# Kernel tuning notes

Measured on AMD Instinct MI355X. Metric: run time of the kernel, lower is better.

## Reference

```python
import jax, jax.numpy as jnp
import numpy as np

B = 128
N = 65536          # total nodes across batched subgraphs
E = 1048576        # total edges
CLIP_DIM = 768
PD = 512           # projection_dim


def setup_inputs() -> dict:
    key = jax.random.key(0)
    ks = jax.random.split(key, 20)
    s = 0.02
    return {
        # CLIP-encoded features (clip encoders treated as upstream feature extractors)
        "image_features": jax.random.normal(ks[0], (B, CLIP_DIM), jnp.float32),
        "text_features": jax.random.normal(ks[1], (B, CLIP_DIM), jnp.float32),
        "answer": jax.random.uniform(ks[2], (B,), jnp.float32),
        # batched subgraph (X_fixed rows already gathered, as in extract_subgraph_batch)
        "x_nodes": jax.random.normal(ks[3], (N, PD), jnp.float32),
        "edge_index": jax.random.randint(ks[4], (2, E), 0, N, jnp.int32),
        "batch_vec": jnp.sort(jax.random.randint(ks[5], (N,), 0, B, jnp.int32)),
        # image/text projections (clip_dim != projection_dim -> Linear)
        "W_img": jax.random.normal(ks[6], (CLIP_DIM, PD), jnp.float32) * s,
        "b_img": jnp.zeros((PD,), jnp.float32),
        "W_txt": jax.random.normal(ks[7], (CLIP_DIM, PD), jnp.float32) * s,
        "b_txt": jnp.zeros((PD,), jnp.float32),
        # implicit classifier: Linear(2*PD, PD) -> ReLU -> Linear(PD, 1)
        "W1": jax.random.normal(ks[8], (2 * PD, PD), jnp.float32) * s,
        "b1": jnp.zeros((PD,), jnp.float32),
        "W2": jax.random.normal(ks[9], (PD, 1), jnp.float32) * s,
        "b2": jnp.zeros((1,), jnp.float32),
        # GCNConv(PD, PD)
        "Wg": jax.random.normal(ks[10], (PD, PD), jnp.float32) * s,
        "bg": jnp.zeros((PD,), jnp.float32),
        # symbolic classifier: Linear(PD, PD) -> ReLU -> Linear(PD, 1)
        "Ws1": jax.random.normal(ks[11], (PD, PD), jnp.float32) * s,
        "bs1": jnp.zeros((PD,), jnp.float32),
        "Ws2": jax.random.normal(ks[12], (PD, 1), jnp.float32) * s,
        "bs2": jnp.zeros((1,), jnp.float32),
    }


def gcn_conv(x, edge_index, W, b):
    """PyG GCNConv: h = W x; add self-loops; sym-normalized sum aggregation."""
    n = x.shape[0]
    h = x @ W                                     # [N, PD] dense GEMM
    loop = jnp.arange(n, dtype=edge_index.dtype)
    src = jnp.concatenate([edge_index[0], loop])  # [E+N]
    dst = jnp.concatenate([edge_index[1], loop])
    deg = jax.ops.segment_sum(jnp.ones_like(dst, dtype=h.dtype), dst, num_segments=n)
    dis = jax.lax.rsqrt(deg)                      # deg >= 1 (self loops)
    norm = dis[src] * dis[dst]                    # [E+N]
    out = jax.ops.segment_sum(h[src] * norm[:, None], dst, num_segments=n)
    return out + b


def reference(image_features, text_features, answer, x_nodes, edge_index, batch_vec,
              W_img, b_img, W_txt, b_txt, W1, b1, W2, b2,
              Wg, bg, Ws1, bs1, Ws2, bs2):
    # ---- implicit branch (MedicalVQAModel.forward) ----
    img = image_features @ W_img + b_img          # [B, PD]
    txt = text_features @ W_txt + b_txt           # [B, PD]
    combined = jnp.concatenate([img, txt], axis=-1)
    h = jax.nn.relu(combined @ W1 + b1)           # dropout p=0.1 inactive (eval)
    y_implicit = (h @ W2 + b2)[:, 0]              # [B]

    # ---- symbolic branch: GCN over batched subgraphs ----
    x = gcn_conv(x_nodes, edge_index, Wg, bg)
    x = jax.nn.relu(x)                            # dropout p=0.8 inactive (eval)
    bv = batch_vec.astype(jnp.int32)
    sums = jax.ops.segment_sum(x, bv, num_segments=B)          # [B, PD]
    cnts = jax.ops.segment_sum(jnp.ones((x.shape[0],), x.dtype), bv, num_segments=B)
    graph_features = sums / jnp.maximum(cnts, 1.0)[:, None]    # global_mean_pool
    hs = jax.nn.relu(graph_features @ Ws1 + bs1)
    y_symbolic = (hs @ Ws2 + bs2)[:, 0]           # [B]

    logits = jnp.maximum(y_implicit, y_symbolic)
    # BCEWithLogits (mean): log(1+e^l) - l*y
    loss = jnp.mean(jnp.logaddexp(0.0, logits) - logits * answer)
    return (logits, loss)
```

## Files before the change

### kernel.cpp

```cpp
#include <hip/hip_runtime.h>
#include <stdint.h>

#define N_NODES 65536
#define N_EDGES 1048576
#define BATCH   128
#define PD      512
#define CLIPD   768

typedef __attribute__((ext_vector_type(4))) float f32x4;
typedef __attribute__((ext_vector_type(2))) float f32x2;
typedef __attribute__((ext_vector_type(4))) int   i32x4;

__device__ __forceinline__ unsigned short f2b(float f) {
    uint32_t u = __float_as_uint(f);
    return (unsigned short)((u + 0x7fffu + ((u >> 16) & 1u)) >> 16);
}

__device__ __forceinline__ uint32_t pk_bf16(float lo, float hi) {
    uint32_t r;
    asm("v_cvt_pk_bf16_f32 %0, %1, %2" : "=v"(r) : "v"(lo), "v"(hi));
    return r;
}

__device__ __forceinline__ uint32_t pk_fp4(float x, float y, float one) {
    uint32_t r = 0;
    asm("v_cvt_scalef32_pk_fp4_f32 %0, %1, %2, %3" : "+v"(r) : "v"(x), "v"(y), "v"(one));
    return r;
}
__device__ __forceinline__ f32x2 upk_fp4(uint32_t b, float one) {
    f32x2 r;
    asm("v_cvt_scalef32_pk_f32_fp4 %0, %1, %2" : "=v"(r) : "v"(b), "v"(one));
    return r;
}

__global__ void k_wgt(const float* __restrict__ Wg, unsigned short* __restrict__ WgT,
                      const int* __restrict__ bv, int* __restrict__ cnts) {
    __shared__ float tile[32][33];
    int kb = blockIdx.x * 32, nb = blockIdx.y * 32;
    int tx = threadIdx.x, ty = threadIdx.y;
    if (kb == 0 && nb == 0) {
        int tid = ty * 32 + tx;
        if (tid < BATCH) {
            int lo = 0, hi = N_NODES;
            while (lo < hi) { int m = (lo + hi) >> 1; if (bv[m] < tid) lo = m + 1; else hi = m; }
            int lo2 = lo, hi2 = N_NODES;
            while (lo2 < hi2) { int m = (lo2 + hi2) >> 1; if (bv[m] < tid + 1) lo2 = m + 1; else hi2 = m; }
            cnts[tid] = lo2 - lo;
        }
    }
    tile[ty][tx] = Wg[(size_t)(kb + ty) * PD + nb + tx];
    __syncthreads();
    WgT[(size_t)(nb + ty) * PD + kb + tx] = f2b(tile[tx][ty]);
}

__global__ void k_deg(const int* __restrict__ ei, int* __restrict__ deg) {
    int e = blockIdx.x * 256 + threadIdx.x;
    atomicAdd(&deg[ei[N_EDGES + e]], 1);
}

__global__ void k_scan(const int* __restrict__ deg, int* __restrict__ row_ptr,
                       float* __restrict__ dis) {
    __shared__ int wsum[16];
    const int t = threadIdx.x;
    const int w = t >> 6, l = t & 63;
    const int base = w * 4096;
    int s = 0;
    for (int i = 0; i < 64; ++i) s += deg[base + i * 64 + l];
#pragma unroll
    for (int off = 1; off < 64; off <<= 1) s += __shfl_xor(s, off);
    if (l == 0) wsum[w] = s;
    __syncthreads();
    int carry = 0;
    for (int i = 0; i < 16; ++i) carry += (i < w) ? wsum[i] : 0;
    int idx = base + l;
    int d = deg[idx];
    for (int i = 0; i < 64; ++i) {
        int dn = 0;
        if (i < 63) dn = deg[idx + 64];
        int v = d;
        int inc = v;
#pragma unroll
        for (int off = 1; off < 64; off <<= 1) {
            int n = __shfl_up(inc, off);
            if (l >= off) inc += n;
        }
        row_ptr[idx] = carry + inc - v;
        dis[idx] = rsqrtf((float)(d + 1));
        carry += __shfl(inc, 63);
        idx += 64;
        d = dn;
    }
    if (t == 1023) row_ptr[N_NODES] = carry;
}

__global__ void k_scatter(const int* __restrict__ ei, const int* __restrict__ row_ptr,
                          int* __restrict__ fill, int* __restrict__ srcs) {
    int e = blockIdx.x * 256 + threadIdx.x;
    int d = ei[N_EDGES + e];
    int pos = row_ptr[d] + atomicAdd(&fill[d], 1);
    srcs[pos] = ei[e];
}

__device__ __forceinline__ void mfma16(f32x4& acc, i32x4 a, i32x4 b) {
    asm("v_mfma_f32_16x16x32_bf16 %0, %1, %2, %0" : "+v"(acc) : "v"(a), "v"(b));
}

__global__ __launch_bounds__(256) void k_gemm(const float* __restrict__ X,
                                              const unsigned short* __restrict__ WgT,
                                              const float* __restrict__ dis,
                                              uint8_t* __restrict__ hn4) {
    __shared__ __align__(16) unsigned short As[128 * 32];
    __shared__ __align__(16) unsigned short Bs[256 * 32];
    const int m0 = blockIdx.x * 128;
    const int n0 = blockIdx.y * 256;
    const int t = threadIdx.x;
    const int lane = t & 63, w = t >> 6;
    const int wr = w >> 1, wc = w & 1;
    const int g = lane >> 4, lr = lane & 15;

    f32x4 acc[4][8] = {};

    for (int k0 = 0; k0 < PD; k0 += 32) {
        __syncthreads();
#pragma unroll
        for (int it = 0; it < 4; ++it) {
            int idx = it * 256 + t;
            int r = idx >> 3, kc = (idx & 7) * 4;
            float4 v = *(const float4*)&X[(size_t)(m0 + r) * PD + k0 + kc];
            uint2 o;
            o.x = pk_bf16(v.x, v.y);
            o.y = pk_bf16(v.z, v.w);
            *(uint2*)&As[r * 32 + kc] = o;
        }
#pragma unroll
        for (int it = 0; it < 4; ++it) {
            int idx = it * 256 + t;
            int r = idx >> 2, kc = (idx & 3) * 8;
            *(uint4*)&Bs[r * 32 + kc] = *(const uint4*)&WgT[(size_t)(n0 + r) * PD + k0 + kc];
        }
        __syncthreads();

        i32x4 a[4], b[8];
#pragma unroll
        for (int i = 0; i < 4; ++i) a[i] = *(const i32x4*)&As[(wr * 64 + i * 16 + lr) * 32 + g * 8];
#pragma unroll
        for (int j = 0; j < 8; ++j) b[j] = *(const i32x4*)&Bs[(wc * 128 + j * 16 + lr) * 32 + g * 8];
#pragma unroll
        for (int i = 0; i < 4; ++i)
#pragma unroll
            for (int j = 0; j < 8; ++j) mfma16(acc[i][j], a[i], b[j]);
    }
    asm volatile("s_nop 7\n s_nop 7\n s_nop 7\n s_nop 7");

    const float one = 1.0f;
#pragma unroll
    for (int i = 0; i < 4; ++i) {
#pragma unroll
        for (int r = 0; r < 4; ++r) {
            int row = m0 + wr * 64 + i * 16 + g * 4 + r;
            float dd = dis[row] * 16.f;
#pragma unroll
            for (int jh = 0; jh < 4; ++jh) {
                float x = acc[i][2 * jh][r] * dd;
                float y = acc[i][2 * jh + 1][r] * dd;
                uint32_t p = pk_fp4(x, y, one);
                hn4[(size_t)row * 256 + (n0 >> 1) + wc * 64 + jh * 16 + lr] = (uint8_t)p;
            }
        }
    }
}

#define NPB 8
__global__ __launch_bounds__(256) void k_agg(const uint8_t* __restrict__ hn4,
                                             const float* __restrict__ dis,
                                             const float* __restrict__ bg,
                                             const int* __restrict__ row_ptr,
                                             const int* __restrict__ srcs,
                                             const int* __restrict__ bv,
                                             float* __restrict__ sums) {
    const int t = threadIdx.x;
    const int c0 = (t >> 4) * 32 + (t & 15);
    const int c1 = c0 + 16;
    const int node0 = blockIdx.x * NPB;
    const float bg0 = bg[c0], bg1 = bg[c1];
    const float one = 1.0f;
    float s0 = 0.f, s1 = 0.f;
    int curb = bv[node0];
    for (int ni = 0; ni < NPB; ++ni) {
        int node = node0 + ni;
        int b = bv[node];
        if (b != curb) {
            atomicAdd(&sums[(size_t)curb * PD + c0], s0);
            atomicAdd(&sums[(size_t)curb * PD + c1], s1);
            s0 = s1 = 0.f;
            curb = b;
        }
        float a0 = 0.f, a1 = 0.f;
        int beg = row_ptr[node], end = row_ptr[node + 1];
        int e = beg;
        for (; e + 16 <= end; e += 16) {
            int sn[16];
#pragma unroll
            for (int q = 0; q < 16; ++q) sn[q] = srcs[e + q];
            uint32_t v[16];
#pragma unroll
            for (int q = 0; q < 16; ++q)
                v[q] = hn4[(size_t)sn[q] * 256 + t];
#pragma unroll
            for (int q = 0; q < 16; ++q) {
                f32x2 f = upk_fp4(v[q], one);
                a0 += f[0];
                a1 += f[1];
            }
        }
        for (; e + 8 <= end; e += 8) {
            int sn[8];
#pragma unroll
            for (int q = 0; q < 8; ++q) sn[q] = srcs[e + q];
            uint32_t v[8];
#pragma unroll
            for (int q = 0; q < 8; ++q)
                v[q] = hn4[(size_t)sn[q] * 256 + t];
#pragma unroll
            for (int q = 0; q < 8; ++q) {
                f32x2 f = upk_fp4(v[q], one);
                a0 += f[0];
                a1 += f[1];
            }
        }
        for (; e < end; ++e) {
            f32x2 f = upk_fp4(hn4[(size_t)srcs[e] * 256 + t], one);
            a0 += f[0];
            a1 += f[1];
        }
        {
            f32x2 f = upk_fp4(hn4[(size_t)node * 256 + t], one);
            a0 += f[0];
            a1 += f[1];
        }
        float dd = dis[node] * 0.0625f;
        a0 = fmaxf(fmaf(a0, dd, bg0), 0.f);
        a1 = fmaxf(fmaf(a1, dd, bg1), 0.f);
        s0 += a0;
        s1 += a1;
    }
    atomicAdd(&sums[(size_t)curb * PD + c0], s0);
    atomicAdd(&sums[(size_t)curb * PD + c1], s1);
}

__device__ __forceinline__ void lin_part_core(const float* __restrict__ a,
                                              const float* __restrict__ wp,
                                              float* __restrict__ P, int slot, int c0) {
    float acc0 = 0.f, acc1 = 0.f, acc2 = 0.f, acc3 = 0.f;
    float acc4 = 0.f, acc5 = 0.f, acc6 = 0.f, acc7 = 0.f;
#pragma unroll 4
    for (int k = 0; k < 256; k += 8) {
        float a0 = a[k + 0], a1 = a[k + 1], a2 = a[k + 2], a3 = a[k + 3];
        float a4 = a[k + 4], a5 = a[k + 5], a6 = a[k + 6], a7 = a[k + 7];
        float2 w0 = *(const float2*)&wp[(size_t)(k + 0) * PD];
        float2 w1 = *(const float2*)&wp[(size_t)(k + 1) * PD];
        float2 w2 = *(const float2*)&wp[(size_t)(k + 2) * PD];
        float2 w3 = *(const float2*)&wp[(size_t)(k + 3) * PD];
        float2 w4 = *(const float2*)&wp[(size_t)(k + 4) * PD];
        float2 w5 = *(const float2*)&wp[(size_t)(k + 5) * PD];
        float2 w6 = *(const float2*)&wp[(size_t)(k + 6) * PD];
        float2 w7 = *(const float2*)&wp[(size_t)(k + 7) * PD];
        acc0 = fmaf(a0, w0.x, acc0); acc1 = fmaf(a0, w0.y, acc1);
        acc2 = fmaf(a1, w1.x, acc2); acc3 = fmaf(a1, w1.y, acc3);
        acc4 = fmaf(a2, w2.x, acc4); acc5 = fmaf(a2, w2.y, acc5);
        acc6 = fmaf(a3, w3.x, acc6); acc7 = fmaf(a3, w3.y, acc7);
        acc0 = fmaf(a4, w4.x, acc0); acc1 = fmaf(a4, w4.y, acc1);
        acc2 = fmaf(a5, w5.x, acc2); acc3 = fmaf(a5, w5.y, acc3);
        acc4 = fmaf(a6, w6.x, acc4); acc5 = fmaf(a6, w6.y, acc5);
        acc6 = fmaf(a7, w7.x, acc6); acc7 = fmaf(a7, w7.y, acc7);
    }
    P[(size_t)slot * PD + c0] = (acc0 + acc2) + (acc4 + acc6);
    P[(size_t)slot * PD + c0 + 1] = (acc1 + acc3) + (acc5 + acc7);
}

__global__ __launch_bounds__(256) void k_lin_part(const float* __restrict__ A,
                                                  const float* __restrict__ W,
                                                  float* __restrict__ P, int K) {
    const int row = blockIdx.x, kc = blockIdx.y, c0 = threadIdx.x * 2;
    lin_part_core(A + (size_t)row * K + kc * 256, W + (size_t)kc * 256 * PD + c0,
                  P, row * 8 + kc, c0);
}

__global__ __launch_bounds__(256) void k_lin_part_it(const float* __restrict__ IMG,
                                                     const float* __restrict__ TXT,
                                                     const float* __restrict__ Wi,
                                                     const float* __restrict__ Wt,
                                                     float* __restrict__ P) {
    const int row = blockIdx.x, kc = blockIdx.y, c0 = threadIdx.x * 2;
    const float* A = (kc < 3) ? IMG : TXT;
    const float* W = (kc < 3) ? Wi : Wt;
    const int sub = (kc < 3) ? kc : kc - 3;
    lin_part_core(A + (size_t)row * CLIPD + sub * 256, W + (size_t)sub * 256 * PD + c0,
                  P, row * 8 + kc, c0);
}

__global__ __launch_bounds__(256) void k_lin_red_it(const float* __restrict__ P,
                                                    const float* __restrict__ bi,
                                                    const float* __restrict__ bt,
                                                    float* __restrict__ C) {
    const int row = blockIdx.x, side = blockIdx.y, c0 = threadIdx.x * 2;
    const float* p = P + ((size_t)row * 8 + side * 3) * PD + c0;
    float r0 = p[0] + p[PD] + p[2 * PD];
    float r1 = p[1] + p[PD + 1] + p[2 * PD + 1];
    const float* bias = side ? bt : bi;
    C[(size_t)row * 1024 + side * PD + c0] = r0 + bias[c0];
    C[(size_t)row * 1024 + side * PD + c0 + 1] = r1 + bias[c0 + 1];
}

__global__ __launch_bounds__(256) void k_reddot(const float* __restrict__ P,
                                                const float* __restrict__ bias,
                                                const float* __restrict__ w2,
                                                const float* __restrict__ b2,
                                                float* __restrict__ y,
                                                int nch, const int* __restrict__ cnts) {
    __shared__ float wred[4];
    const int row = blockIdx.x;
    const int t = threadIdx.x;
    const int c0 = t * 2;
    const float* p = P + (size_t)row * 8 * PD + c0;
    float r0 = p[0], r1 = p[1];
    if (nch > 1) { r0 += p[PD];     r1 += p[PD + 1]; }
    if (nch > 2) { r0 += p[2 * PD]; r1 += p[2 * PD + 1]; }
    if (nch > 3) { r0 += p[3 * PD]; r1 += p[3 * PD + 1]; }
    float s = 1.f;
    if (cnts) s = 1.f / fmaxf((float)cnts[row], 1.f);
    r0 = fmaxf(fmaf(r0, s, bias[c0]), 0.f);
    r1 = fmaxf(fmaf(r1, s, bias[c0 + 1]), 0.f);
    float partial = fmaf(r0, w2[c0], r1 * w2[c0 + 1]);
#pragma unroll
    for (int off = 32; off; off >>= 1) partial += __shfl_down(partial, off);
    if ((t & 63) == 0) wred[t >> 6] = partial;
    __syncthreads();
    if (t == 0) y[row] = (wred[0] + wred[1]) + (wred[2] + wred[3]) + b2[0];
}

__global__ void k_final(const float* __restrict__ yi, const float* __restrict__ ys,
                        const float* __restrict__ ans, float* __restrict__ out) {
    __shared__ float red[128];
    int t = threadIdx.x;
    float l = fmaxf(yi[t], ys[t]);
    out[t] = l;
    float li = fmaxf(l, 0.f) + log1pf(expf(-fabsf(l))) - l * ans[t];
    red[t] = li;
    __syncthreads();
    for (int off = 64; off; off >>= 1) {
        if (t < off) red[t] += red[t + off];
        __syncthreads();
    }
    if (t == 0) out[BATCH] = red[0] / (float)BATCH;
}

extern "C" void kernel_launch(void* const* d_in, const int* in_sizes, int n_in,
                              void* d_out, int out_size, void* d_ws, size_t ws_size,
                              hipStream_t stream) {
    const float* image_features = (const float*)d_in[0];
    const float* text_features  = (const float*)d_in[1];
    const float* answer         = (const float*)d_in[2];
    const float* x_nodes        = (const float*)d_in[3];
    const int*   edge_index     = (const int*)d_in[4];
    const int*   batch_vec      = (const int*)d_in[5];
    const float* W_img = (const float*)d_in[6];
    const float* b_img = (const float*)d_in[7];
    const float* W_txt = (const float*)d_in[8];
    const float* b_txt = (const float*)d_in[9];
    const float* W1  = (const float*)d_in[10];
    const float* b1  = (const float*)d_in[11];
    const float* W2  = (const float*)d_in[12];
    const float* b2  = (const float*)d_in[13];
    const float* Wg  = (const float*)d_in[14];
    const float* bg  = (const float*)d_in[15];
    const float* Ws1 = (const float*)d_in[16];
    const float* bs1 = (const float*)d_in[17];
    const float* Ws2 = (const float*)d_in[18];
    const float* bs2 = (const float*)d_in[19];
    float* out = (float*)d_out;

    char* base = (char*)d_ws;
    size_t cur = 0;
    auto alloc = [&](size_t bytes) -> void* {
        void* r = base + cur;
        cur = (cur + bytes + 255) & ~(size_t)255;
        return r;
    };
    unsigned short* WgT = (unsigned short*)alloc((size_t)PD * PD * 2);
    uint8_t* hn4   = (uint8_t*)alloc((size_t)N_NODES * 256);
    int*   deg     = (int*)alloc((size_t)N_NODES * 4);
    float* dis     = (float*)alloc((size_t)N_NODES * 4);
    int*   row_ptr = (int*)alloc((size_t)(N_NODES + 1) * 4);
    int*   fill    = (int*)alloc((size_t)N_NODES * 4);
    int*   srcs    = (int*)alloc((size_t)N_EDGES * 4);
    float* sums    = (float*)alloc((size_t)BATCH * PD * 4);
    int*   cnts    = (int*)alloc((size_t)BATCH * 4);
    float* Ppart   = (float*)alloc((size_t)BATCH * 8 * PD * 4);
    float* combined = (float*)alloc((size_t)BATCH * 1024 * 4);
    float* yi      = (float*)alloc((size_t)BATCH * 4);
    float* ys      = (float*)alloc((size_t)BATCH * 4);

    hipMemsetAsync(deg, 0, (size_t)N_NODES * 4, stream);
    hipMemsetAsync(fill, 0, (size_t)N_NODES * 4, stream);
    hipMemsetAsync(sums, 0, (size_t)BATCH * PD * 4, stream);

    hipLaunchKernelGGL(k_wgt, dim3(16, 16), dim3(32, 32), 0, stream, Wg, WgT, batch_vec, cnts);
    hipLaunchKernelGGL(k_deg, dim3(4096), dim3(256), 0, stream, edge_index, deg);
    hipLaunchKernelGGL(k_scan, dim3(1), dim3(1024), 0, stream, deg, row_ptr, dis);
    hipLaunchKernelGGL(k_scatter, dim3(4096), dim3(256), 0, stream, edge_index, row_ptr, fill, srcs);
    hipLaunchKernelGGL(k_gemm, dim3(N_NODES / 128, PD / 256), dim3(256), 0, stream,
                       x_nodes, WgT, dis, hn4);
    hipLaunchKernelGGL(k_agg, dim3(N_NODES / NPB), dim3(256), 0, stream,
                       hn4, dis, bg, row_ptr, srcs, batch_vec, sums);

    hipLaunchKernelGGL(k_lin_part_it, dim3(BATCH, 6), dim3(256), 0, stream,
                       image_features, text_features, W_img, W_txt, Ppart);
    hipLaunchKernelGGL(k_lin_red_it, dim3(BATCH, 2), dim3(256), 0, stream,
                       Ppart, b_img, b_txt, combined);
    hipLaunchKernelGGL(k_lin_part, dim3(BATCH, 4), dim3(256), 0, stream,
                       combined, W1, Ppart, 1024);
    hipLaunchKernelGGL(k_reddot, dim3(BATCH), dim3(256), 0, stream,
                       Ppart, b1, W2, b2, yi, 4, (const int*)nullptr);

    hipLaunchKernelGGL(k_lin_part, dim3(BATCH, 2), dim3(256), 0, stream,
                       sums, Ws1, Ppart, PD);
    hipLaunchKernelGGL(k_reddot, dim3(BATCH), dim3(256), 0, stream,
                       Ppart, bs1, Ws2, bs2, ys, 2, cnts);

    hipLaunchKernelGGL(k_final, dim3(1), dim3(128), 0, stream, yi, ys, answer, out);
}
```

Baseline: 366.8 us.

## Swizzle GEMM tile order, load B via global_load_lds, prefetch edge indices

The GEMM now remaps block indices in a swizzled order so that concurrently running blocks share row tiles of X. It also moves the WgT tile straight from global memory into LDS with global_load_lds instead of staging it through registers. In the aggregation kernel, the next 16 source indices are loaded while the current 16 gathers are in flight, so the index loads overlap with the feature gathers. This adds register pressure and hardcodes the grid shape (512 row blocks) in the swizzle.

After: 359.7 us. No clear change (-1.9%).

```diff
diff --git a/kernel.cpp b/kernel.cpp
--- a/kernel.cpp
+++ b/kernel.cpp
@@ -31,6 +31,11 @@
     f32x2 r;
     asm("v_cvt_scalef32_pk_f32_fp4 %0, %1, %2" : "=v"(r) : "v"(b), "v"(one));
     return r;
+}
+
+__device__ __forceinline__ void gl_lds16(const unsigned short* g, unsigned short* l) {
+    __builtin_amdgcn_global_load_lds((const __attribute__((address_space(1))) void*)g,
+                                     (__attribute__((address_space(3))) void*)l, 16, 0, 0);
 }
 
 __global__ void k_wgt(const float* __restrict__ Wg, unsigned short* __restrict__ WgT,
@@ -111,8 +116,10 @@
                                               uint8_t* __restrict__ hn4) {
     __shared__ __align__(16) unsigned short As[128 * 32];
     __shared__ __align__(16) unsigned short Bs[256 * 32];
-    const int m0 = blockIdx.x * 128;
-    const int n0 = blockIdx.y * 256;
+    const int lin = blockIdx.x + blockIdx.y * 512;
+    const int swz = (lin & 7) * 128 + (lin >> 3);
+    const int m0 = (swz & 511) * 128;
+    const int n0 = (swz >> 9) * 256;
     const int t = threadIdx.x;
     const int lane = t & 63, w = t >> 6;
     const int wr = w >> 1, wc = w & 1;
@@ -136,7 +143,7 @@
         for (int it = 0; it < 4; ++it) {
             int idx = it * 256 + t;
             int r = idx >> 2, kc = (idx & 3) * 8;
-            *(uint4*)&Bs[r * 32 + kc] = *(const uint4*)&WgT[(size_t)(n0 + r) * PD + k0 + kc];
+            gl_lds16(&WgT[(size_t)(n0 + r) * PD + k0 + kc], &Bs[idx * 8]);
         }
         __syncthreads();
 
@@ -198,19 +205,37 @@
         float a0 = 0.f, a1 = 0.f;
         int beg = row_ptr[node], end = row_ptr[node + 1];
         int e = beg;
-        for (; e + 16 <= end; e += 16) {
+        if (e + 16 <= end) {
             int sn[16];
 #pragma unroll
             for (int q = 0; q < 16; ++q) sn[q] = srcs[e + q];
-            uint32_t v[16];
-#pragma unroll
-            for (int q = 0; q < 16; ++q)
-                v[q] = hn4[(size_t)sn[q] * 256 + t];
-#pragma unroll
-            for (int q = 0; q < 16; ++q) {
-                f32x2 f = upk_fp4(v[q], one);
-                a0 += f[0];
-                a1 += f[1];
+            for (; e + 32 <= end; e += 16) {
+                int sn2[16];
+#pragma unroll
+                for (int q = 0; q < 16; ++q) sn2[q] = srcs[e + 16 + q];
+                uint32_t v[16];
+#pragma unroll
+                for (int q = 0; q < 16; ++q) v[q] = hn4[(size_t)sn[q] * 256 + t];
+#pragma unroll
+                for (int q = 0; q < 16; ++q) {
+                    f32x2 f = upk_fp4(v[q], one);
+                    a0 += f[0];
+                    a1 += f[1];
+                }
+#pragma unroll
+                for (int q = 0; q < 16; ++q) sn[q] = sn2[q];
+            }
+            {
+                uint32_t v[16];
+#pragma unroll
+                for (int q = 0; q < 16; ++q) v[q] = hn4[(size_t)sn[q] * 256 + t];
+#pragma unroll
+                for (int q = 0; q < 16; ++q) {
+                    f32x2 f = upk_fp4(v[q], one);
+                    a0 += f[0];
+                    a1 += f[1];
+                }
+                e += 16;
             }
         }
         for (; e + 8 <= end; e += 8) {
```
